# Kernel tuning notes

Measured on AMD Instinct MI355X. Metric: run time of the kernel, lower is better.

Reference implementation:

```python
import jax, jax.numpy as jnp
import numpy as np

N = 500_000          # n_nodes
E = 16_000_000       # n_edges (avg degree 32)
F0 = 3               # INIT_DIM, input feature dim
H = 32               # hidden units
N_MID = 6            # num_layers=8 -> 1 first + 6 mid + 1 last
ALPHA = 0.9          # self.ALHPA in the original


def setup_inputs() -> dict:
    key = jax.random.key(0)
    ks = jax.random.split(key, 10)
    s = 0.1  # glorot-ish scale for tiny dims
    x = jax.random.normal(ks[0], (N, F0), jnp.float32)
    rows = jax.random.randint(ks[1], (E,), 0, N, jnp.int32)
    cols = jax.random.randint(ks[2], (E,), 0, N, jnp.int32)
    # normalized adjacency values (positive, small, like D^-1/2 A D^-1/2)
    vals = jax.random.uniform(ks[3], (E,), jnp.float32) * 0.1
    w_init0 = jax.random.normal(ks[4], (F0, F0), jnp.float32) * s
    w_x0 = jax.random.normal(ks[5], (F0, H), jnp.float32) * s
    w_init_mid = jax.random.normal(ks[6], (N_MID, F0, H), jnp.float32) * s
    w_x_mid = jax.random.normal(ks[7], (N_MID, H, H), jnp.float32) * s
    w_init_last = jax.random.normal(ks[8], (F0, H), jnp.float32) * s
    w_x_last = jax.random.normal(ks[9], (H, 1), jnp.float32) * s
    return dict(x=x, rows=rows, cols=cols, vals=vals,
                w_init0=w_init0, w_x0=w_x0,
                w_init_mid=w_init_mid, w_x_mid=w_x_mid,
                w_init_last=w_init_last, w_x_last=w_x_last)


def _spmm(rows, cols, vals, x):
    # sparse [N,N] @ dense [N,F] via COO gather + segment scatter-add
    return jax.ops.segment_sum(vals[:, None] * x[cols], rows, num_segments=N)


def _layer(h, x0, rows, cols, vals, w_init, w_x, act):
    agg = _spmm(rows, cols, vals, h)                       # [N, F]
    blend = ALPHA * agg + (1.0 - ALPHA) * (x0 @ w_init)    # alpha-blended residual
    return act(blend @ w_x)                                # dense transform + activation


def reference(x, rows, cols, vals, w_init0, w_x0, w_init_mid, w_x_mid,
              w_init_last, w_x_last):
    x0 = x
    h = _layer(x, x0, rows, cols, vals, w_init0, w_x0, jax.nn.relu)
    for i in range(N_MID):  # fixed small loop over structurally distinct layers
        h = _layer(h, x0, rows, cols, vals, w_init_mid[i], w_x_mid[i], jax.nn.relu)
    return _layer(h, x0, rows, cols, vals, w_init_last, w_x_last, jax.nn.sigmoid)
```

## Files before the change

kernel.cpp:

```cpp
#include <hip/hip_runtime.h>
#include <hip/hip_fp16.h>

#define NN 500000
#define NE 16000000
#define HD 32
#define NMID 6
#define F0 3

#define RPB 1024
#define NBUK ((NN + RPB - 1) / RPB)
#define GRID_P 2048
#define EBLK ((NE + GRID_P - 1) / GRID_P)

static constexpr float ALPHA = 0.9f;
static constexpr float OMA = 1.0f - 0.9f;

__global__ void prep_pack(const float* __restrict__ w_init_mid,
                          const float* __restrict__ w_x_mid,
                          const float* __restrict__ w_init_last,
                          const float* __restrict__ w_x_last,
                          float4* __restrict__ wpk,
                          float2* __restrict__ wc2,
                          float* __restrict__ wcl) {
    int t = blockIdx.x * 512 + threadIdx.x;
    if (t < 5 * 256) {
        int i = t >> 8, r = t & 255, k = r >> 4, f = r & 15;
        const float* W = w_x_mid + (size_t)(i + 1) * HD * HD;
        wpk[t] = make_float4(W[(2 * k) * HD + 2 * f], W[(2 * k) * HD + 2 * f + 1],
                             W[(2 * k + 1) * HD + 2 * f], W[(2 * k + 1) * HD + 2 * f + 1]);
    } else if (t < 5 * 256 + NMID * 48) {
        int r = t - 1280;
        int i = r / 48, rr = r % 48, k = rr >> 4, f = rr & 15;
        const float* wi = w_init_mid + (size_t)i * F0 * HD;
        const float* wx = w_x_mid + (size_t)i * HD * HD;
        float a = 0.f, b = 0.f;
        for (int j = 0; j < HD; ++j) {
            a += wi[k * HD + j] * wx[j * HD + 2 * f];
            b += wi[k * HD + j] * wx[j * HD + 2 * f + 1];
        }
        wc2[r] = make_float2(OMA * a, OMA * b);
    } else if (t < 1280 + NMID * 48 + F0) {
        int k = t - (1280 + NMID * 48);
        float a = 0.f;
        for (int j = 0; j < HD; ++j) a += w_init_last[k * HD + j] * w_x_last[j];
        wcl[k] = OMA * a;
    }
}

__global__ void bucket_hist(const int* __restrict__ rows, int* __restrict__ cnt) {
    __shared__ int lh[512];
    int tid = threadIdx.x;
    lh[tid] = 0;
    __syncthreads();
    int e0 = blockIdx.x * EBLK;
    int e1 = min(e0 + EBLK, NE);
    for (int e = e0 + tid; e < e1; e += 512)
        atomicAdd(&lh[rows[e] >> 10], 1);
    __syncthreads();
    if (tid < NBUK && lh[tid]) atomicAdd(&cnt[tid], lh[tid]);
}

__global__ void scan_buckets(int* __restrict__ cnt) {
    __shared__ int s[512];
    int tid = threadIdx.x;
    int v = (tid < NBUK) ? cnt[tid] : 0;
    s[tid] = v;
    __syncthreads();
    for (int off = 1; off < 512; off <<= 1) {
        int t = (tid >= off) ? s[tid - off] : 0;
        __syncthreads();
        s[tid] += t;
        __syncthreads();
    }
    if (tid < NBUK) cnt[tid] = s[tid] - v;
}

__global__ void p1_scatter(const int* __restrict__ rows, const int* __restrict__ cols,
                           const float* __restrict__ vals, int* __restrict__ tail,
                           int2* __restrict__ tmp) {
    __shared__ int lh[512], gb[512], lp[512];
    int tid = threadIdx.x;
    lh[tid] = 0;
    __syncthreads();
    int e0 = blockIdx.x * EBLK;
    int e1 = min(e0 + EBLK, NE);
    for (int e = e0 + tid; e < e1; e += 512)
        atomicAdd(&lh[rows[e] >> 10], 1);
    __syncthreads();
    if (tid < NBUK && lh[tid]) gb[tid] = atomicAdd(&tail[tid], lh[tid]);
    lp[tid] = 0;
    __syncthreads();
    for (int e = e0 + tid; e < e1; e += 512) {
        int r = rows[e];
        int b = r >> 10;
        int loc = atomicAdd(&lp[b], 1);
        int pos = gb[b] + loc;
        tmp[pos] = make_int2(((r & (RPB - 1)) << 19) | cols[e], __float_as_int(vals[e]));
    }
}

__global__ void __launch_bounds__(1024) p2_csr(const int* __restrict__ tail,
                                               const int2* __restrict__ tmp,
                                               int* __restrict__ rp,
                                               int2* __restrict__ es) {
    __shared__ int a[RPB];
    __shared__ int tl[RPB];
    int b = blockIdx.x, tid = threadIdx.x;
    int estart = (b == 0) ? 0 : tail[b - 1];
    int eend = tail[b];
    a[tid] = 0;
    __syncthreads();
    for (int e = estart + tid; e < eend; e += RPB)
        atomicAdd(&a[tmp[e].x >> 19], 1);
    __syncthreads();
    int myc = a[tid];
    for (int off = 1; off < RPB; off <<= 1) {
        int t = (tid >= off) ? a[tid - off] : 0;
        __syncthreads();
        a[tid] += t;
        __syncthreads();
    }
    int rend = estart + a[tid];
    tl[tid] = rend - myc;
    int grow = b * RPB + tid;
    if (grow < NN) rp[grow] = rend;
    __syncthreads();
    for (int e = estart + tid; e < eend; e += RPB) {
        int2 t = tmp[e];
        int rl = t.x >> 19;
        int pos = atomicAdd(&tl[rl], 1);
        es[pos] = make_int2(t.x & 0x7FFFF, t.y);
    }
}

__global__ void layer1_fused(const int* __restrict__ rp, const int2* __restrict__ es,
                             const float* __restrict__ x0, const float* __restrict__ w_init0,
                             const float* __restrict__ w_x0, const float* __restrict__ w_x1,
                             unsigned int* __restrict__ gh_out) {
    int tid = blockIdx.x * 256 + threadIdx.x;
    int n = tid >> 5, f = tid & 31;
    if (n >= NN) return;
    int s = (n == 0) ? 0 : rp[n - 1];
    int e_end = rp[n];
    float a0 = 0.f, a1 = 0.f, a2 = 0.f;
    for (int e = s + f; e < e_end; e += 32) {
        int2 ev = es[e];
        int c = ev.x; float v = __int_as_float(ev.y);
        a0 += v * x0[c * 3 + 0];
        a1 += v * x0[c * 3 + 1];
        a2 += v * x0[c * 3 + 2];
    }
    #pragma unroll
    for (int m = 16; m >= 1; m >>= 1) {
        a0 += __shfl_xor(a0, m, 32);
        a1 += __shfl_xor(a1, m, 32);
        a2 += __shfl_xor(a2, m, 32);
    }
    float p0 = x0[n * 3 + 0], p1 = x0[n * 3 + 1], p2 = x0[n * 3 + 2];
    float b0 = ALPHA * a0 + OMA * (p0 * w_init0[0] + p1 * w_init0[3] + p2 * w_init0[6]);
    float b1 = ALPHA * a1 + OMA * (p0 * w_init0[1] + p1 * w_init0[4] + p2 * w_init0[7]);
    float b2 = ALPHA * a2 + OMA * (p0 * w_init0[2] + p1 * w_init0[5] + p2 * w_init0[8]);
    float h = fmaxf(b0 * w_x0[f] + b1 * w_x0[HD + f] + b2 * w_x0[2 * HD + f], 0.f);
    float o = 0.f;
    #pragma unroll
    for (int k = 0; k < HD; ++k) o += __shfl(h, k, 32) * w_x1[k * HD + f];
    o *= ALPHA;
    float o_hi = __shfl_down(o, 1, 32);
    if ((f & 1) == 0) {
        __half2 hp;
        hp.x = __float2half_rn(o);
        hp.y = __float2half_rn(o_hi);
        gh_out[(size_t)n * 16 + (f >> 1)] = *(unsigned int*)&hp;
    }
}

template<int MODE>
__global__ void mid_fused(const int* __restrict__ rp, const int2* __restrict__ es,
                          const unsigned int* __restrict__ gh_in,
                          const float* __restrict__ x0,
                          const float2* __restrict__ wc2,
                          const float4* __restrict__ wpk,
                          const float* __restrict__ w_last,
                          float* __restrict__ g1_out,
                          unsigned int* __restrict__ gh_out) {
    int tid = blockIdx.x * 256 + threadIdx.x;
    int n = tid >> 4, f = tid & 15;
    if (n >= NN) return;
    int grp = threadIdx.x >> 4;
    __shared__ int2 stage[16][16];
    int s = (n == 0) ? 0 : rp[n - 1];
    int e_end = rp[n];
    float acc0 = 0.f, acc1 = 0.f;
    for (int base = s; base < e_end; base += 16) {
        int e = base + f;
        int2 ev = (e < e_end) ? es[e] : make_int2(0, 0);
        stage[grp][f] = ev;
        int2 ee[16];
        #pragma unroll
        for (int k = 0; k < 16; ++k) ee[k] = stage[grp][k];
        unsigned int gw[16];
        #pragma unroll
        for (int k = 0; k < 16; ++k) gw[k] = gh_in[(ee[k].x << 4) + f];
        #pragma unroll
        for (int k = 0; k < 16; ++k) {
            float v = __int_as_float(ee[k].y);
            __half2 h2 = *(__half2*)&gw[k];
            float2 gf = __half22float2(h2);
            acc0 = fmaf(v, gf.x, acc0);
            acc1 = fmaf(v, gf.y, acc1);
        }
    }
    float xa = x0[n * 3 + 0], xb = x0[n * 3 + 1], xc = x0[n * 3 + 2];
    float2 w0 = wc2[f], w1 = wc2[16 + f], w2 = wc2[32 + f];
    float h0 = fmaxf(xa * w0.x + xb * w1.x + xc * w2.x + acc0, 0.f);
    float h1 = fmaxf(xa * w0.y + xb * w1.y + xc * w2.y + acc1, 0.f);
    if (MODE == 0) {
        float o0 = 0.f, o1 = 0.f;
        #pragma unroll
        for (int k = 0; k < 16; ++k) {
            float ha = __shfl(h0, k, 16);
            float hb = __shfl(h1, k, 16);
            float4 w = wpk[k * 16 + f];
            o0 += ha * w.x + hb * w.z;
            o1 += ha * w.y + hb * w.w;
        }
        __half2 hp;
        hp.x = __float2half_rn(ALPHA * o0);
        hp.y = __float2half_rn(ALPHA * o1);
        gh_out[(size_t)n * 16 + f] = *(unsigned int*)&hp;
    } else {
        float2 wl = ((const float2*)w_last)[f];
        float t = h0 * wl.x + h1 * wl.y;
        #pragma unroll
        for (int m = 8; m >= 1; m >>= 1) t += __shfl_xor(t, m, 16);
        if (f == 0) g1_out[n] = ALPHA * t;
    }
}

__global__ void last_fused(const int* __restrict__ rp, const int2* __restrict__ es,
                           const float* __restrict__ g1, const float* __restrict__ x0,
                           const float* __restrict__ wcL, float* __restrict__ out) {
    int tid = blockIdx.x * 256 + threadIdx.x;
    int n = tid >> 5, f = tid & 31;
    if (n >= NN) return;
    int s = (n == 0) ? 0 : rp[n - 1];
    int e_end = rp[n];
    float acc = 0.f;
    for (int e = s + f; e < e_end; e += 32) {
        int2 ev = es[e];
        acc += __int_as_float(ev.y) * g1[ev.x];
    }
    #pragma unroll
    for (int m = 16; m >= 1; m >>= 1) acc += __shfl_xor(acc, m, 32);
    if (f == 0) {
        float z = x0[n * 3 + 0] * wcL[0] + x0[n * 3 + 1] * wcL[1] + x0[n * 3 + 2] * wcL[2] + acc;
        out[n] = 1.f / (1.f + __expf(-z));
    }
}

__global__ void fb_spmm_f3(const int* __restrict__ rows, const int* __restrict__ cols,
                           const float* __restrict__ vals, const float* __restrict__ x,
                           float* __restrict__ agg3) {
    int e = blockIdx.x * blockDim.x + threadIdx.x;
    if (e >= NE) return;
    int r = rows[e], c = cols[e];
    float v = vals[e];
    atomicAdd(&agg3[r * 3 + 0], v * x[c * 3 + 0]);
    atomicAdd(&agg3[r * 3 + 1], v * x[c * 3 + 1]);
    atomicAdd(&agg3[r * 3 + 2], v * x[c * 3 + 2]);
}
__global__ void fb_epilogue1(const float* __restrict__ agg3, const float* __restrict__ x0,
                             const float* __restrict__ w_init0, const float* __restrict__ w_x0,
                             const float* __restrict__ w_x_next, float* __restrict__ g_out) {
    int tid = blockIdx.x * blockDim.x + threadIdx.x;
    int n = tid >> 5, f = tid & 31;
    if (n >= NN) return;
    float a0 = agg3[n * 3 + 0], a1 = agg3[n * 3 + 1], a2 = agg3[n * 3 + 2];
    float p0 = x0[n * 3 + 0], p1 = x0[n * 3 + 1], p2 = x0[n * 3 + 2];
    float b0 = ALPHA * a0 + OMA * (p0 * w_init0[0] + p1 * w_init0[3] + p2 * w_init0[6]);
    float b1 = ALPHA * a1 + OMA * (p0 * w_init0[1] + p1 * w_init0[4] + p2 * w_init0[7]);
    float b2 = ALPHA * a2 + OMA * (p0 * w_init0[2] + p1 * w_init0[5] + p2 * w_init0[8]);
    float h = fmaxf(b0 * w_x0[f] + b1 * w_x0[HD + f] + b2 * w_x0[2 * HD + f], 0.f);
    float acc = 0.f;
    #pragma unroll
    for (int k = 0; k < HD; ++k) acc += __shfl(h, k, 32) * w_x_next[k * HD + f];
    g_out[n * HD + f] = ALPHA * acc;
}
__global__ void fb_seed_mid(const float* __restrict__ x0, const float* __restrict__ wc,
                            float* __restrict__ agg) {
    int tid = blockIdx.x * blockDim.x + threadIdx.x;
    int n = tid >> 5, f = tid & 31;
    if (n >= NN) return;
    agg[n * HD + f] = x0[n * 3 + 0] * wc[f] + x0[n * 3 + 1] * wc[HD + f] + x0[n * 3 + 2] * wc[2 * HD + f];
}
__global__ void fb_spmm_f32(const int* __restrict__ rows, const int* __restrict__ cols,
                            const float* __restrict__ vals, const float* __restrict__ g,
                            float* __restrict__ agg) {
    int tid = blockIdx.x * blockDim.x + threadIdx.x;
    int e = tid >> 5, f = tid & 31;
    if (e >= NE) return;
    atomicAdd(&agg[rows[e] * HD + f], vals[e] * g[cols[e] * HD + f]);
}
__global__ void fb_epilogue_mid(const float* __restrict__ agg, const float* __restrict__ w_x_next,
                                float* __restrict__ g_out) {
    int tid = blockIdx.x * blockDim.x + threadIdx.x;
    int n = tid >> 5, f = tid & 31;
    if (n >= NN) return;
    float h = fmaxf(agg[n * HD + f], 0.f);
    float acc = 0.f;
    #pragma unroll
    for (int k = 0; k < HD; ++k) acc += __shfl(h, k, 32) * w_x_next[k * HD + f];
    g_out[n * HD + f] = ALPHA * acc;
}
__global__ void fb_epilogue_to1(const float* __restrict__ agg, const float* __restrict__ w_x_last,
                                float* __restrict__ g1) {
    int tid = blockIdx.x * blockDim.x + threadIdx.x;
    int n = tid >> 5, f = tid & 31;
    if (n >= NN) return;
    float v = fmaxf(agg[n * HD + f], 0.f) * w_x_last[f];
    #pragma unroll
    for (int m = 16; m >= 1; m >>= 1) v += __shfl_xor(v, m, 32);
    if (f == 0) g1[n] = ALPHA * v;
}
__global__ void fb_seed_last(const float* __restrict__ x0, const float* __restrict__ wcL,
                             float* __restrict__ aggL) {
    int n = blockIdx.x * blockDim.x + threadIdx.x;
    if (n >= NN) return;
    aggL[n] = x0[n * 3 + 0] * wcL[0] + x0[n * 3 + 1] * wcL[1] + x0[n * 3 + 2] * wcL[2];
}
__global__ void fb_spmm_f1(const int* __restrict__ rows, const int* __restrict__ cols,
                           const float* __restrict__ vals, const float* __restrict__ g1,
                           float* __restrict__ aggL) {
    int e = blockIdx.x * blockDim.x + threadIdx.x;
    if (e >= NE) return;
    atomicAdd(&aggL[rows[e]], vals[e] * g1[cols[e]]);
}
__global__ void fb_final_sigmoid(const float* __restrict__ aggL, float* __restrict__ out) {
    int n = blockIdx.x * blockDim.x + threadIdx.x;
    if (n >= NN) return;
    out[n] = 1.f / (1.f + __expf(-aggL[n]));
}
__global__ void fb_prep_weights(const float* __restrict__ w_init_mid,
                                const float* __restrict__ w_x_mid,
                                const float* __restrict__ w_init_last,
                                const float* __restrict__ w_x_last,
                                float* __restrict__ wc_mid,
                                float* __restrict__ wc_last) {
    int t = threadIdx.x;
    if (t < NMID * F0 * HD) {
        int i = t / (F0 * HD);
        int r = t - i * (F0 * HD);
        int k = r / HD, f = r % HD;
        const float* wi = w_init_mid + (size_t)i * F0 * HD;
        const float* wx = w_x_mid + (size_t)i * HD * HD;
        float acc = 0.f;
        for (int j = 0; j < HD; ++j) acc += wi[k * HD + j] * wx[j * HD + f];
        wc_mid[t] = OMA * acc;
    } else if (t < NMID * F0 * HD + F0) {
        int k = t - NMID * F0 * HD;
        float acc = 0.f;
        for (int j = 0; j < HD; ++j) acc += w_init_last[k * HD + j] * w_x_last[j];
        wc_last[k] = OMA * acc;
    }
}

extern "C" void kernel_launch(void* const* d_in, const int* in_sizes, int n_in,
                              void* d_out, int out_size, void* d_ws, size_t ws_size,
                              hipStream_t stream) {
    const float* x           = (const float*)d_in[0];
    const int*   rows        = (const int*)d_in[1];
    const int*   cols        = (const int*)d_in[2];
    const float* vals        = (const float*)d_in[3];
    const float* w_init0     = (const float*)d_in[4];
    const float* w_x0        = (const float*)d_in[5];
    const float* w_init_mid  = (const float*)d_in[6];
    const float* w_x_mid     = (const float*)d_in[7];
    const float* w_init_last = (const float*)d_in[8];
    const float* w_x_last    = (const float*)d_in[9];
    float* out = (float*)d_out;

    const int B = 256;
    const int gridE   = NE / B;
    const int gridN32 = (NN * 32 + B - 1) / B;
    const int gridN16 = (NN * 16 + B - 1) / B;
    const int gridN   = (NN + B - 1) / B;

    const size_t SZ_ES = (size_t)NE * 8;
    const size_t SZ_G  = (size_t)NN * HD * 4;
    const size_t SZ_RP = (size_t)NN * 4;
    const size_t NEED  = SZ_ES + 2 * SZ_G + SZ_RP + 4096 + 4096;

    if (ws_size >= NEED) {
        char* base = (char*)d_ws;
        int2*  es   = (int2*)base;
        char*  reg2 = base + SZ_ES;
        int2*  tmp  = (int2*)reg2;
        unsigned int* gA = (unsigned int*)reg2;
        unsigned int* gB = (unsigned int*)(reg2 + (size_t)NN * HD * 2);
        float* g1   = (float*)(reg2 + (size_t)2 * NN * HD * 2);
        float4* wpk = (float4*)(reg2 + 70000000);
        float2* wc2 = (float2*)(reg2 + 70000000 + 5 * 256 * 16);
        float*  wcl = (float*)(reg2 + 70000000 + 5 * 256 * 16 + NMID * 48 * 8);
        int*   rp   = (int*)(base + SZ_ES + 2 * SZ_G);
        int*   bkt  = (int*)(base + SZ_ES + 2 * SZ_G + SZ_RP);

        hipMemsetAsync(bkt, 0, NBUK * sizeof(int), stream);
        bucket_hist<<<GRID_P, 512, 0, stream>>>(rows, bkt);
        scan_buckets<<<1, 512, 0, stream>>>(bkt);
        p1_scatter<<<GRID_P, 512, 0, stream>>>(rows, cols, vals, bkt, tmp);
        p2_csr<<<NBUK, RPB, 0, stream>>>(bkt, tmp, rp, es);

        prep_pack<<<4, 512, 0, stream>>>(w_init_mid, w_x_mid, w_init_last, w_x_last,
                                         wpk, wc2, wcl);

        layer1_fused<<<gridN32, B, 0, stream>>>(rp, es, x, w_init0, w_x0, w_x_mid, gA);
        unsigned int* gin = gA; unsigned int* gout = gB;
        for (int i = 0; i < NMID - 1; ++i) {
            mid_fused<0><<<gridN16, B, 0, stream>>>(rp, es, gin, x, wc2 + i * 48,
                                                    wpk + i * 256, nullptr, nullptr, gout);
            unsigned int* t = gin; gin = gout; gout = t;
        }
        mid_fused<1><<<gridN16, B, 0, stream>>>(rp, es, gin, x, wc2 + 5 * 48,
                                                nullptr, w_x_last, g1, nullptr);
        last_fused<<<gridN32, B, 0, stream>>>(rp, es, g1, x, wcl, out);
    } else {
        char* ws = (char*)d_ws;
        float* g      = (float*)ws;
        float* agg    = (float*)(ws + SZ_G);
        float* wc_mid = (float*)(ws + 2 * SZ_G);
        float* wc_last = wc_mid + NMID * F0 * HD;

        fb_prep_weights<<<1, 1024, 0, stream>>>(w_init_mid, w_x_mid, w_init_last, w_x_last,
                                                wc_mid, wc_last);
        hipMemsetAsync(agg, 0, (size_t)NN * 3 * sizeof(float), stream);
        fb_spmm_f3<<<gridE, B, 0, stream>>>(rows, cols, vals, x, agg);
        fb_epilogue1<<<gridN32, B, 0, stream>>>(agg, x, w_init0, w_x0, w_x_mid, g);
        const int gridE32 = (int)(((size_t)NE * 32) / B);
        for (int i = 0; i < NMID; ++i) {
            fb_seed_mid<<<gridN32, B, 0, stream>>>(x, wc_mid + i * F0 * HD, agg);
            fb_spmm_f32<<<gridE32, B, 0, stream>>>(rows, cols, vals, g, agg);
            if (i < NMID - 1)
                fb_epilogue_mid<<<gridN32, B, 0, stream>>>(agg, w_x_mid + (size_t)(i + 1) * HD * HD, g);
            else
                fb_epilogue_to1<<<gridN32, B, 0, stream>>>(agg, w_x_last, g);
        }
        fb_seed_last<<<gridN, B, 0, stream>>>(x, wc_last, agg);
        fb_spmm_f1<<<gridE, B, 0, stream>>>(rows, cols, vals, g, agg);
        fb_final_sigmoid<<<gridN, B, 0, stream>>>(agg, out);
    }
}
```

Before: 2.469 ms.

## Split CSR edges into SoA and store edge values as fp16, pack x as half

```diff
diff --git a/kernel.cpp b/kernel.cpp
--- a/kernel.cpp
+++ b/kernel.cpp
@@ -9,11 +9,20 @@
 
 #define RPB 1024
 #define NBUK ((NN + RPB - 1) / RPB)
-#define GRID_P 2048
+#define GRID_P 512
 #define EBLK ((NE + GRID_P - 1) / GRID_P)
 
 static constexpr float ALPHA = 0.9f;
 static constexpr float OMA = 1.0f - 0.9f;
+
+static __device__ __forceinline__ unsigned short f2h_bits(float v) {
+    __half h = __float2half_rn(v);
+    return *reinterpret_cast<unsigned short*>(&h);
+}
+static __device__ __forceinline__ float h_bits2f(unsigned short b) {
+    __half h = *reinterpret_cast<__half*>(&b);
+    return __half2float(h);
+}
 
 __global__ void prep_pack(const float* __restrict__ w_init_mid,
                           const float* __restrict__ w_x_mid,
@@ -47,6 +56,15 @@
     }
 }
 
+__global__ void prep_xh(const float* __restrict__ x, uint2* __restrict__ xh) {
+    int n = blockIdx.x * 256 + threadIdx.x;
+    if (n >= NN) return;
+    __half2 lo = __floats2half2_rn(x[n * 3 + 0], x[n * 3 + 1]);
+    __half2 hi = __floats2half2_rn(x[n * 3 + 2], 0.f);
+    xh[n] = make_uint2(*reinterpret_cast<unsigned int*>(&lo),
+                       *reinterpret_cast<unsigned int*>(&hi));
+}
+
 __global__ void bucket_hist(const int* __restrict__ rows, int* __restrict__ cnt) {
     __shared__ int lh[512];
     int tid = threadIdx.x;
@@ -77,7 +95,7 @@
 
 __global__ void p1_scatter(const int* __restrict__ rows, const int* __restrict__ cols,
                            const float* __restrict__ vals, int* __restrict__ tail,
-                           int2* __restrict__ tmp) {
+                           int* __restrict__ tmp_ci, unsigned short* __restrict__ tmp_vh) {
     __shared__ int lh[512], gb[512], lp[512];
     int tid = threadIdx.x;
     lh[tid] = 0;
@@ -95,14 +113,17 @@
         int b = r >> 10;
         int loc = atomicAdd(&lp[b], 1);
         int pos = gb[b] + loc;
-        tmp[pos] = make_int2(((r & (RPB - 1)) << 19) | cols[e], __float_as_int(vals[e]));
+        tmp_ci[pos] = ((r & (RPB - 1)) << 19) | cols[e];
+        tmp_vh[pos] = f2h_bits(vals[e]);
     }
 }
 
 __global__ void __launch_bounds__(1024) p2_csr(const int* __restrict__ tail,
-                                               const int2* __restrict__ tmp,
+                                               const int* __restrict__ tmp_ci,
+                                               const unsigned short* __restrict__ tmp_vh,
                                                int* __restrict__ rp,
-                                               int2* __restrict__ es) {
+                                               int* __restrict__ escol,
+                                               unsigned short* __restrict__ esvalh) {
     __shared__ int a[RPB];
     __shared__ int tl[RPB];
     int b = blockIdx.x, tid = threadIdx.x;
@@ -111,7 +132,7 @@
     a[tid] = 0;
     __syncthreads();
     for (int e = estart + tid; e < eend; e += RPB)
-        atomicAdd(&a[tmp[e].x >> 19], 1);
+        atomicAdd(&a[tmp_ci[e] >> 19], 1);
     __syncthreads();
     int myc = a[tid];
     for (int off = 1; off < RPB; off <<= 1) {
@@ -126,14 +147,17 @@
     if (grow < NN) rp[grow] = rend;
     __syncthreads();
     for (int e = estart + tid; e < eend; e += RPB) {
-        int2 t = tmp[e];
-        int rl = t.x >> 19;
+        int ci = tmp_ci[e];
+        int rl = ci >> 19;
         int pos = atomicAdd(&tl[rl], 1);
-        es[pos] = make_int2(t.x & 0x7FFFF, t.y);
-    }
-}
-
-__global__ void layer1_fused(const int* __restrict__ rp, const int2* __restrict__ es,
+        escol[pos] = ci & 0x7FFFF;
+        esvalh[pos] = tmp_vh[e];
+    }
+}
+
+__global__ void layer1_fused(const int* __restrict__ rp, const int* __restrict__ escol,
+                             const unsigned short* __restrict__ esvalh,
+                             const uint2* __restrict__ xh,
                              const float* __restrict__ x0, const float* __restrict__ w_init0,
                              const float* __restrict__ w_x0, const float* __restrict__ w_x1,
                              unsigned int* __restrict__ gh_out) {
@@ -144,11 +168,16 @@
     int e_end = rp[n];
     float a0 = 0.f, a1 = 0.f, a2 = 0.f;
     for (int e = s + f; e < e_end; e += 32) {
-        int2 ev = es[e];
-        int c = ev.x; float v = __int_as_float(ev.y);
-        a0 += v * x0[c * 3 + 0];
-        a1 += v * x0[c * 3 + 1];
-        a2 += v * x0[c * 3 + 2];
+        int c = escol[e];
+        float v = h_bits2f(esvalh[e]);
+        uint2 xw = xh[c];
+        __half2 lo = *reinterpret_cast<__half2*>(&xw.x);
+        __half2 hi = *reinterpret_cast<__half2*>(&xw.y);
+        float2 flo = __half22float2(lo);
+        float2 fhi = __half22float2(hi);
+        a0 = fmaf(v, flo.x, a0);
+        a1 = fmaf(v, flo.y, a1);
+        a2 = fmaf(v, fhi.x, a2);
     }
     #pragma unroll
     for (int m = 16; m >= 1; m >>= 1) {
@@ -170,12 +199,13 @@
         __half2 hp;
         hp.x = __float2half_rn(o);
         hp.y = __float2half_rn(o_hi);
-        gh_out[(size_t)n * 16 + (f >> 1)] = *(unsigned int*)&hp;
+        gh_out[(size_t)n * 16 + (f >> 1)] = *reinterpret_cast<unsigned int*>(&hp);
     }
 }
 
 template<int MODE>
-__global__ void mid_fused(const int* __restrict__ rp, const int2* __restrict__ es,
+__global__ void mid_fused(const int* __restrict__ rp, const int* __restrict__ escol,
+                          const unsigned short* __restrict__ esvalh,
                           const unsigned int* __restrict__ gh_in,
                           const float* __restrict__ x0,
                           const float2* __restrict__ wc2,
@@ -187,24 +217,27 @@
     int n = tid >> 4, f = tid & 15;
     if (n >= NN) return;
     int grp = threadIdx.x >> 4;
-    __shared__ int2 stage[16][16];
+    __shared__ int stage_c[16][16];
+    __shared__ int stage_v[16][16];
     int s = (n == 0) ? 0 : rp[n - 1];
     int e_end = rp[n];
     float acc0 = 0.f, acc1 = 0.f;
     for (int base = s; base < e_end; base += 16) {
         int e = base + f;
-        int2 ev = (e < e_end) ? es[e] : make_int2(0, 0);
-        stage[grp][f] = ev;
-        int2 ee[16];
+        int c = 0, vb = 0;
+        if (e < e_end) { c = escol[e]; vb = esvalh[e]; }
+        stage_c[grp][f] = c;
+        stage_v[grp][f] = vb;
+        int cc[16], vv[16];
         #pragma unroll
-        for (int k = 0; k < 16; ++k) ee[k] = stage[grp][k];
+        for (int k = 0; k < 16; ++k) { cc[k] = stage_c[grp][k]; vv[k] = stage_v[grp][k]; }
         unsigned int gw[16];
         #pragma unroll
-        for (int k = 0; k < 16; ++k) gw[k] = gh_in[(ee[k].x << 4) + f];
+        for (int k = 0; k < 16; ++k) gw[k] = gh_in[((size_t)cc[k] << 4) + f];
         #pragma unroll
         for (int k = 0; k < 16; ++k) {
-            float v = __int_as_float(ee[k].y);
-            __half2 h2 = *(__half2*)&gw[k];
+            float v = h_bits2f((unsigned short)vv[k]);
+            __half2 h2 = *reinterpret_cast<__half2*>(&gw[k]);
             float2 gf = __half22float2(h2);
             acc0 = fmaf(v, gf.x, acc0);
             acc1 = fmaf(v, gf.y, acc1);
@@ -227,7 +260,7 @@
         __half2 hp;
         hp.x = __float2half_rn(ALPHA * o0);
         hp.y = __float2half_rn(ALPHA * o1);
-        gh_out[(size_t)n * 16 + f] = *(unsigned int*)&hp;
+        gh_out[(size_t)n * 16 + f] = *reinterpret_cast<unsigned int*>(&hp);
     } else {
         float2 wl = ((const float2*)w_last)[f];
         float t = h0 * wl.x + h1 * wl.y;
@@ -237,7 +270,8 @@
     }
 }
 
-__global__ void last_fused(const int* __restrict__ rp, const int2* __restrict__ es,
+__global__ void last_fused(const int* __restrict__ rp, const int* __restrict__ escol,
+                           const unsigned short* __restrict__ esvalh,
                            const float* __restrict__ g1, const float* __restrict__ x0,
                            const float* __restrict__ wcL, float* __restrict__ out) {
     int tid = blockIdx.x * 256 + threadIdx.x;
@@ -247,8 +281,7 @@
     int e_end = rp[n];
     float acc = 0.f;
     for (int e = s + f; e < e_end; e += 32) {
-        int2 ev = es[e];
-        acc += __int_as_float(ev.y) * g1[ev.x];
+        acc = fmaf(h_bits2f(esvalh[e]), g1[escol[e]], acc);
     }
     #pragma unroll
     for (int m = 16; m >= 1; m >>= 1) acc += __shfl_xor(acc, m, 32);
@@ -392,37 +425,42 @@
 
     if (ws_size >= NEED) {
         char* base = (char*)d_ws;
-        int2*  es   = (int2*)base;
-        char*  reg2 = base + SZ_ES;
-        int2*  tmp  = (int2*)reg2;
+        int* escol = (int*)base;
+        unsigned short* esvalh = (unsigned short*)(base + (size_t)NE * 4);
+        char* reg2 = base + SZ_ES;
+        int* tmp_ci = (int*)reg2;
+        unsigned short* tmp_vh = (unsigned short*)(reg2 + (size_t)NE * 4);
         unsigned int* gA = (unsigned int*)reg2;
         unsigned int* gB = (unsigned int*)(reg2 + (size_t)NN * HD * 2);
-        float* g1   = (float*)(reg2 + (size_t)2 * NN * HD * 2);
+        float* g1  = (float*)(reg2 + (size_t)2 * NN * HD * 2);
+        uint2* xh  = (uint2*)(reg2 + (size_t)2 * NN * HD * 2 + (size_t)NN * 4);
         float4* wpk = (float4*)(reg2 + 70000000);
         float2* wc2 = (float2*)(reg2 + 70000000 + 5 * 256 * 16);
         float*  wcl = (float*)(reg2 + 70000000 + 5 * 256 * 16 + NMID * 48 * 8);
-        int*   rp   = (int*)(base + SZ_ES + 2 * SZ_G);
-        int*   bkt  = (int*)(base + SZ_ES + 2 * SZ_G + SZ_RP);
+        int* rp  = (int*)(base + SZ_ES + 2 * SZ_G);
+        int* bkt = (int*)(base + SZ_ES + 2 * SZ_G + SZ_RP);
 
         hipMemsetAsync(bkt, 0, NBUK * sizeof(int), stream);
         bucket_hist<<<GRID_P, 512, 0, stream>>>(rows, bkt);
         scan_buckets<<<1, 512, 0, stream>>>(bkt);
-        p1_scatter<<<GRID_P, 512, 0, stream>>>(rows, cols, vals, bkt, tmp);
-        p2_csr<<<NBUK, RPB, 0, stream>>>(bkt, tmp, rp, es);
+        p1_scatter<<<GRID_P, 512, 0, stream>>>(rows, cols, vals, bkt, tmp_ci, tmp_vh);
+        p2_csr<<<NBUK, RPB, 0, stream>>>(bkt, tmp_ci, tmp_vh, rp, escol, esvalh);
 
         prep_pack<<<4, 512, 0, stream>>>(w_init_mid, w_x_mid, w_init_last, w_x_last,
                                          wpk, wc2, wcl);
-
-        layer1_fused<<<gridN32, B, 0, stream>>>(rp, es, x, w_init0, w_x0, w_x_mid, gA);
+        prep_xh<<<gridN, B, 0, stream>>>(x, xh);
+
+        layer1_fused<<<gridN32, B, 0, stream>>>(rp, escol, esvalh, xh, x,
+                                                w_init0, w_x0, w_x_mid, gA);
         unsigned int* gin = gA; unsigned int* gout = gB;
         for (int i = 0; i < NMID - 1; ++i) {
-            mid_fused<0><<<gridN16, B, 0, stream>>>(rp, es, gin, x, wc2 + i * 48,
+            mid_fused<0><<<gridN16, B, 0, stream>>>(rp, escol, esvalh, gin, x, wc2 + i * 48,
                                                     wpk + i * 256, nullptr, nullptr, gout);
             unsigned int* t = gin; gin = gout; gout = t;
         }
-        mid_fused<1><<<gridN16, B, 0, stream>>>(rp, es, gin, x, wc2 + 5 * 48,
+        mid_fused<1><<<gridN16, B, 0, stream>>>(rp, escol, esvalh, gin, x, wc2 + 5 * 48,
                                                 nullptr, w_x_last, g1, nullptr);
-        last_fused<<<gridN32, B, 0, stream>>>(rp, es, g1, x, wcl, out);
+        last_fused<<<gridN32, B, 0, stream>>>(rp, escol, esvalh, g1, x, wcl, out);
     } else {
         char* ws = (char*)d_ws;
         float* g      = (float*)ws;
```

After: 2.930 ms. +18.7%, slower.
